# Performance work log

Measured on AMD Instinct MI355X. Metric: run time of the kernel, lower is better.

## Reference

```python
import jax, jax.numpy as jnp
import numpy as np

L, B, S, D, H = 6, 2, 2048, 512, 8
DH = D // H
FF = 4 * D
EPS = 1e-5


def setup_inputs() -> dict:
    key = jax.random.key(0)
    ks = jax.random.split(key, 10)
    w = lambda k, shape: jax.random.normal(k, shape, jnp.float32) * 0.02
    return {
        "query": jax.random.normal(ks[0], (B, S, D), jnp.float32),
        "key": jax.random.normal(ks[1], (B, S, D), jnp.float32),
        "query_mask": jnp.ones((B, S), jnp.int32),
        "key_mask": jnp.ones((B, S), jnp.int32),
        # per-layer stacked params; conv1d(kernel=1) == linear with weight [out,in]
        "Wq": w(ks[2], (L, D, D)), "bq": jnp.zeros((L, D), jnp.float32),
        "Wk": w(ks[3], (L, D, D)), "bk": jnp.zeros((L, D), jnp.float32),
        "Wv": w(ks[4], (L, D, D)), "bv": jnp.zeros((L, D), jnp.float32),
        "Wo": w(ks[5], (L, D, D)), "bo": jnp.zeros((L, D), jnp.float32),
        "ln1_g": jnp.ones((L, D), jnp.float32), "ln1_b": jnp.zeros((L, D), jnp.float32),
        "ff_w1": w(ks[6], (L, FF, D)), "ff_b1": jnp.zeros((L, FF), jnp.float32),
        "ff_w2": w(ks[7], (L, D, FF)), "ff_b2": jnp.zeros((L, D), jnp.float32),
        "ln2_g": jnp.ones((L, D), jnp.float32), "ln2_b": jnp.zeros((L, D), jnp.float32),
    }


def _layer_norm(x, g, b):
    m = jnp.mean(x, axis=-1, keepdims=True)
    v = jnp.mean(jnp.square(x - m), axis=-1, keepdims=True)
    return (x - m) * jax.lax.rsqrt(v + EPS) * g + b


def reference(query, key, query_mask, key_mask,
              Wq, bq, Wk, bk, Wv, bv, Wo, bo,
              ln1_g, ln1_b, ff_w1, ff_b1, ff_w2, ff_b2, ln2_g, ln2_b):
    b_, s_, d_ = query.shape
    kpad = (key_mask == 0)[:, None, None, :]          # [B,1,1,K]
    qm = query_mask.astype(query.dtype)[:, :, None]    # [B,S,1]
    x = query
    for i in range(L):
        # QKV projections (conv1d kernel-size-1 == linear), split heads -> [B,H,S,DH]
        def split(t):
            return t.reshape(b_, s_, H, DH).transpose(0, 2, 1, 3)
        q = split(x @ Wq[i].T + bq[i]) * (float(DH) ** -0.5)
        k = split(key @ Wk[i].T + bk[i])
        v = split(key @ Wv[i].T + bv[i])
        attn = jnp.einsum('bhqd,bhkd->bhqk', q, k)
        attn = jnp.where(kpad, -jnp.inf, attn)
        attn = jax.nn.softmax(attn, axis=-1)
        o = jnp.einsum('bhqk,bhkd->bhqd', attn, v)
        o = o.transpose(0, 2, 1, 3).reshape(b_, s_, H * DH)
        o = (o @ Wo[i].T + bo[i]) * qm                 # output proj + query mask
        x = _layer_norm(o + x, ln1_g[i], ln1_b[i])
        h = jax.nn.leaky_relu(x @ ff_w1[i].T + ff_b1[i], 0.01)
        f = (h @ ff_w2[i].T + ff_b2[i]) * qm           # FFN mask on output
        x = _layer_norm(f + x, ln2_g[i], ln2_b[i])
    return x
```

## Files before the change

kernel.cpp:

```cpp
#include <hip/hip_runtime.h>
#include <stdint.h>

constexpr int LAYERS = 6;
constexpr int Bc = 2, Sc = 2048, Dc = 512, Hc = 8, DHc = 64, FFc = 2048;
constexpr int Mc = Bc * Sc;
constexpr int NS = 2;
constexpr int KCHUNK = Sc / NS;

typedef __attribute__((ext_vector_type(8))) __bf16 bf16x8;
typedef __attribute__((ext_vector_type(4))) __bf16 bf16x4;
typedef __attribute__((ext_vector_type(4))) float f32x4;

__device__ __forceinline__ void async_ld16(const void* g, void* lds) {
  __builtin_amdgcn_global_load_lds(
      (const __attribute__((address_space(1))) uint32_t*)g,
      (__attribute__((address_space(3))) uint32_t*)lds, 16, 0, 0);
}

__global__ __launch_bounds__(256) void cvt_kernel(const float* __restrict__ in,
                                                  __bf16* __restrict__ out, int n) {
  int i = (blockIdx.x * 256 + threadIdx.x) * 4;
  if (i + 4 > n) return;
  const float4 v = *(const float4*)(in + i);
  bf16x4 o;
  o[0] = (__bf16)v.x; o[1] = (__bf16)v.y; o[2] = (__bf16)v.z; o[3] = (__bf16)v.w;
  *(bf16x4*)(out + i) = o;
}

template <int BM, int BN, int WM, int WN, int EPI>
__global__ __launch_bounds__(256) void gemm_bt(
    const __bf16* __restrict__ A, const __bf16* __restrict__ W,
    const float* __restrict__ bias, const float* __restrict__ bias2,
    float* __restrict__ outf, __bf16* __restrict__ outb,
    __bf16* __restrict__ outb2, const int* __restrict__ rmask, float scale,
    int M, int N, int K) {
  constexpr int BK = 32;
  __shared__ __bf16 As[2][BM * BK];
  __shared__ __bf16 Bs[2][BN * BK];
  const int tid = threadIdx.x;
  const int l15 = tid & 15;
  const int lg = (tid & 63) >> 4;
  const int w = tid >> 6;
  const int wm = w >> 1, wn = w & 1;
  const int tm = blockIdx.y * BM;
  const int tn = blockIdx.x * BN;
  const __bf16* Ap = A + (size_t)tm * K;
  const __bf16* Wp = W + (size_t)tn * K;
  f32x4 acc[WM][WN] = {};

  auto stage = [&](int k0, int bf) {
#pragma unroll
    for (int c = 0; c < BM * 4 / 256; ++c) {
      int cc = c * 256 + tid;
      async_ld16(Ap + (size_t)(cc >> 2) * K + k0 + (cc & 3) * 8, &As[bf][cc * 8]);
    }
#pragma unroll
    for (int c = 0; c < BN * 4 / 256; ++c) {
      int cc = c * 256 + tid;
      async_ld16(Wp + (size_t)(cc >> 2) * K + k0 + (cc & 3) * 8, &Bs[bf][cc * 8]);
    }
  };

  const int nk = K / BK;
  stage(0, 0);
  __syncthreads();
  int buf = 0;
  for (int t = 0; t < nk; ++t) {
    if (t + 1 < nk) stage((t + 1) * BK, buf ^ 1);
    bf16x8 af[WM], bfr[WN];
#pragma unroll
    for (int i = 0; i < WM; ++i)
      af[i] = *(const bf16x8*)&As[buf][(wm * WM * 16 + i * 16 + l15) * BK + lg * 8];
#pragma unroll
    for (int j = 0; j < WN; ++j)
      bfr[j] = *(const bf16x8*)&Bs[buf][(wn * WN * 16 + j * 16 + l15) * BK + lg * 8];
#pragma unroll
    for (int i = 0; i < WM; ++i)
#pragma unroll
      for (int j = 0; j < WN; ++j)
        acc[i][j] = __builtin_amdgcn_mfma_f32_16x16x32_bf16(af[i], bfr[j], acc[i][j], 0, 0, 0);
    __syncthreads();
    buf ^= 1;
  }

#pragma unroll
  for (int i = 0; i < WM; ++i) {
#pragma unroll
    for (int j = 0; j < WN; ++j) {
      const int n = tn + wn * WN * 16 + j * 16 + l15;
      float bv;
      if constexpr (EPI == 6) {
        int lyr = n >> 10, w1 = n & 1023, p = w1 >> 9, d = w1 & 511;
        bv = (p ? bias2 : bias)[lyr * 512 + d];
      } else {
        bv = bias[n];
      }
#pragma unroll
      for (int r = 0; r < 4; ++r) {
        const int m = tm + wm * WM * 16 + i * 16 + lg * 4 + r;
        float v = acc[i][j][r] + bv;
        if constexpr (EPI == 1) {
          int b = m >> 11, s = m & (Sc - 1);
          int h = n >> 6, dh = n & 63;
          outb[(((size_t)(b * Hc + h)) * Sc + s) * DHc + dh] = (__bf16)(v * scale);
        } else if constexpr (EPI == 3) {
          outf[(size_t)m * N + n] = v * (float)rmask[m];
        } else if constexpr (EPI == 4) {
          float lv = v > 0.f ? v : 0.01f * v;
          outb[(size_t)m * N + n] = (__bf16)lv;
        } else if constexpr (EPI == 6) {
          int b = m >> 11, s = m & (Sc - 1);
          int lyr = n >> 10, w1 = n & 1023, p = w1 >> 9, d = w1 & 511;
          int h = d >> 6, dh = d & 63;
          if (p == 0)
            outb[((((size_t)(lyr * Bc + b) * Hc + h)) * Sc + s) * DHc + dh] = (__bf16)v;
          else
            outb2[((((size_t)(lyr * Bc + b) * Hc + h)) * DHc + dh) * Sc + s] = (__bf16)v;
        }
      }
    }
  }
}

__global__ __launch_bounds__(256, 4) void attn_kernel(
    const __bf16* __restrict__ q, const __bf16* __restrict__ k,
    const __bf16* __restrict__ vt, const int* __restrict__ kmask,
    __bf16* __restrict__ Opart, float* __restrict__ mpart,
    float* __restrict__ lpart) {
  const int bh = blockIdx.y;
  const int b = bh >> 3;
  const int z = blockIdx.z;
  const int w = threadIdx.x >> 6;
  const int l = threadIdx.x & 63;
  const int l15 = l & 15;
  const int lg = l >> 4;
  const int tid = threadIdx.x;
  const int qbase = blockIdx.x * 64 + w * 16;
  const int k0 = z * KCHUNK;

  const __bf16* qp = q + ((size_t)bh * Sc + qbase) * DHc;
  const __bf16* kp = k + (size_t)bh * Sc * DHc;
  const __bf16* vp = vt + (size_t)bh * DHc * Sc;

  bf16x8 qf[2];
  qf[0] = *(const bf16x8*)(qp + l15 * DHc + lg * 8);
  qf[1] = *(const bf16x8*)(qp + l15 * DHc + 32 + lg * 8);

  bf16x8 onesf;
#pragma unroll
  for (int i = 0; i < 8; ++i) onesf[i] = (__bf16)1.0f;

  f32x4 oacc[4] = {};
  f32x4 lacc = {};
  float mr[4] = {-1e30f, -1e30f, -1e30f, -1e30f};

  __shared__ __bf16 Ks[2][4096];
  __shared__ __bf16 Vs[2][4096];
  __shared__ __bf16 P[4][1024];

  auto stage = [&](int t, int bf) {
    const int kt = k0 + t * 64;
#pragma unroll
    for (int ii = 0; ii < 2; ++ii) {
      int i = ii * 256 + tid;
      int r = i >> 3;
      int bsrc = (i & 7) ^ (r & 7);
      async_ld16(kp + (size_t)(kt + r) * DHc + bsrc * 8, &Ks[bf][i * 8]);
      async_ld16(vp + (size_t)r * Sc + kt + bsrc * 8, &Vs[bf][i * 8]);
    }
  };

  stage(0, 0);
  __syncthreads();

  constexpr int NT = KCHUNK / 64;
  int buf = 0;
  for (int t = 0; t < NT; ++t) {
    const int kt = k0 + t * 64;
    if (t + 1 < NT) stage(t + 1, buf ^ 1);

    f32x4 sacc[4] = {};
#pragma unroll
    for (int kf = 0; kf < 2; ++kf) {
#pragma unroll
      for (int cb = 0; cb < 4; ++cb) {
        int row = cb * 16 + l15;
        bf16x8 kfr = *(const bf16x8*)&Ks[buf][row * 64 + (((kf * 4 + lg) ^ (row & 7)) * 8)];
        sacc[cb] = __builtin_amdgcn_mfma_f32_16x16x32_bf16(qf[kf], kfr, sacc[cb], 0, 0, 0);
      }
    }
#pragma unroll
    for (int cb = 0; cb < 4; ++cb) {
      if (kmask[b * Sc + kt + cb * 16 + l15] == 0) {
        sacc[cb][0] = -1e30f; sacc[cb][1] = -1e30f;
        sacc[cb][2] = -1e30f; sacc[cb][3] = -1e30f;
      }
    }
    float fac[4];
#pragma unroll
    for (int j = 0; j < 4; ++j) {
      float mx = fmaxf(fmaxf(sacc[0][j], sacc[1][j]), fmaxf(sacc[2][j], sacc[3][j]));
#pragma unroll
      for (int d = 1; d < 16; d <<= 1) mx = fmaxf(mx, __shfl_xor(mx, d, 64));
      float mn = fmaxf(mr[j], mx);
      fac[j] = __expf(mr[j] - mn);
      mr[j] = mn;
    }
#pragma unroll
    for (int cb = 0; cb < 4; ++cb)
#pragma unroll
      for (int j = 0; j < 4; ++j) sacc[cb][j] = __expf(sacc[cb][j] - mr[j]);
#pragma unroll
    for (int j = 0; j < 4; ++j) lacc[j] *= fac[j];
#pragma unroll
    for (int db = 0; db < 4; ++db)
#pragma unroll
      for (int j = 0; j < 4; ++j) oacc[db][j] *= fac[j];

#pragma unroll
    for (int cb = 0; cb < 4; ++cb)
#pragma unroll
      for (int j = 0; j < 4; ++j) {
        int qrow = lg * 4 + j;
        P[w][qrow * 64 + ((cb * 16 + l15) ^ ((qrow & 7) << 3))] = (__bf16)sacc[cb][j];
      }
#pragma unroll
    for (int kf = 0; kf < 2; ++kf) {
      bf16x8 pf = *(const bf16x8*)&P[w][l15 * 64 + (((kf * 4 + lg) ^ (l15 & 7)) * 8)];
      lacc = __builtin_amdgcn_mfma_f32_16x16x32_bf16(pf, onesf, lacc, 0, 0, 0);
#pragma unroll
      for (int db = 0; db < 4; ++db) {
        int row = db * 16 + l15;
        bf16x8 vf = *(const bf16x8*)&Vs[buf][row * 64 + (((kf * 4 + lg) ^ (row & 7)) * 8)];
        oacc[db] = __builtin_amdgcn_mfma_f32_16x16x32_bf16(pf, vf, oacc[db], 0, 0, 0);
      }
    }
    __syncthreads();
    buf ^= 1;
  }

  const size_t obase = (((size_t)(z * Bc * Hc + bh)) * Sc + qbase) * DHc;
#pragma unroll
  for (int db = 0; db < 4; ++db)
#pragma unroll
    for (int j = 0; j < 4; ++j)
      Opart[obase + (size_t)(lg * 4 + j) * DHc + db * 16 + l15] = (__bf16)oacc[db][j];
  if (l15 == 0) {
#pragma unroll
    for (int j = 0; j < 4; ++j) {
      int row = (z * Bc * Hc + bh) * Sc + qbase + lg * 4 + j;
      mpart[row] = mr[j];
      lpart[row] = lacc[j];
    }
  }
}

__global__ __launch_bounds__(256) void attn_combine(
    const __bf16* __restrict__ Opart, const float* __restrict__ mpart,
    const float* __restrict__ lpart, __bf16* __restrict__ out) {
  int t = blockIdx.x * 256 + threadIdx.x;
  int d = t & 63;
  int row = t >> 6;
  int bh = row >> 11, s = row & (Sc - 1);
  constexpr int RSTRIDE = Bc * Hc * Sc;
  float m0 = mpart[row], m1 = mpart[RSTRIDE + row];
  float l0 = lpart[row], l1 = lpart[RSTRIDE + row];
  float M = fmaxf(m0, m1);
  float e0 = __expf(m0 - M), e1 = __expf(m1 - M);
  float denom = e0 * l0 + e1 * l1;
  float o0 = (float)Opart[(size_t)row * DHc + d];
  float o1 = (float)Opart[((size_t)RSTRIDE + row) * DHc + d];
  float o = (e0 * o0 + e1 * o1) / denom;
  int b = bh >> 3, h = bh & 7;
  out[(((size_t)b * Sc + s)) * Dc + h * DHc + d] = (__bf16)o;
}

__global__ __launch_bounds__(256) void add_ln_kernel(
    const float* __restrict__ res, const float* __restrict__ xin,
    const float* __restrict__ g, const float* __restrict__ bb,
    float* __restrict__ xo, __bf16* __restrict__ xbo) {
  const int row = blockIdx.x;
  const int tid = threadIdx.x;
  const float* rp = res + (size_t)row * Dc;
  const float* xp = xin + (size_t)row * Dc;
  float v0 = rp[tid] + xp[tid];
  float v1 = rp[tid + 256] + xp[tid + 256];
  float s = v0 + v1;
#pragma unroll
  for (int d = 1; d < 64; d <<= 1) s += __shfl_xor(s, d, 64);
  __shared__ float red[4], red2[4];
  if ((tid & 63) == 0) red[tid >> 6] = s;
  __syncthreads();
  float mean = (red[0] + red[1] + red[2] + red[3]) * (1.0f / Dc);
  float d0 = v0 - mean, d1 = v1 - mean;
  float qq = d0 * d0 + d1 * d1;
#pragma unroll
  for (int d = 1; d < 64; d <<= 1) qq += __shfl_xor(qq, d, 64);
  if ((tid & 63) == 0) red2[tid >> 6] = qq;
  __syncthreads();
  float var = (red2[0] + red2[1] + red2[2] + red2[3]) * (1.0f / Dc);
  float rs = rsqrtf(var + 1e-5f);
  float o0 = d0 * rs * g[tid] + bb[tid];
  float o1 = d1 * rs * g[tid + 256] + bb[tid + 256];
  xo[(size_t)row * Dc + tid] = o0;
  xo[(size_t)row * Dc + tid + 256] = o1;
  xbo[(size_t)row * Dc + tid] = (__bf16)o0;
  xbo[(size_t)row * Dc + tid + 256] = (__bf16)o1;
}

extern "C" void kernel_launch(void* const* d_in, const int* in_sizes, int n_in,
                              void* d_out, int out_size, void* d_ws, size_t ws_size,
                              hipStream_t stream) {
  (void)in_sizes; (void)n_in; (void)out_size; (void)ws_size;
  const float* query = (const float*)d_in[0];
  const float* key   = (const float*)d_in[1];
  const int* qmask   = (const int*)d_in[2];
  const int* kmask   = (const int*)d_in[3];
  const float* Wq = (const float*)d_in[4];
  const float* bq = (const float*)d_in[5];
  const float* Wk = (const float*)d_in[6];
  const float* bk = (const float*)d_in[7];
  const float* Wv = (const float*)d_in[8];
  const float* bv = (const float*)d_in[9];
  const float* Wo = (const float*)d_in[10];
  const float* bo = (const float*)d_in[11];
  const float* ln1g = (const float*)d_in[12];
  const float* ln1b = (const float*)d_in[13];
  const float* fw1 = (const float*)d_in[14];
  const float* fb1 = (const float*)d_in[15];
  const float* fw2 = (const float*)d_in[16];
  const float* fb2 = (const float*)d_in[17];
  const float* ln2g = (const float*)d_in[18];
  const float* ln2b = (const float*)d_in[19];

  char* ws = (char*)d_ws;
  size_t off = 0;
  auto carve = [&](size_t bytes) -> void* {
    void* p = ws + off;
    off += (bytes + 255) & ~(size_t)255;
    return p;
  };
  float* x_f    = (float*)carve((size_t)Mc * Dc * 4);
  float* tmp_f  = (float*)carve((size_t)Mc * Dc * 4);
  __bf16* x_b   = (__bf16*)carve((size_t)Mc * Dc * 2);
  __bf16* key_b = (__bf16*)carve((size_t)Mc * Dc * 2);
  __bf16* q_b   = (__bf16*)carve((size_t)Mc * Dc * 2);
  __bf16* at_b  = (__bf16*)carve((size_t)Mc * Dc * 2);
  __bf16* h_b   = (__bf16*)carve((size_t)Mc * FFc * 2);
  __bf16* k_all = (__bf16*)carve((size_t)LAYERS * Mc * Dc * 2);
  __bf16* vt_all= (__bf16*)carve((size_t)LAYERS * Mc * Dc * 2);
  __bf16* wq_b  = (__bf16*)carve((size_t)LAYERS * Dc * Dc * 2);
  __bf16* wkv_b = (__bf16*)carve((size_t)LAYERS * 2 * Dc * Dc * 2);
  __bf16* wo_b  = (__bf16*)carve((size_t)LAYERS * Dc * Dc * 2);
  __bf16* w1_b  = (__bf16*)carve((size_t)LAYERS * FFc * Dc * 2);
  __bf16* w2_b  = (__bf16*)carve((size_t)LAYERS * Dc * FFc * 2);
  float* ml_f   = (float*)carve((size_t)NS * Bc * Hc * Sc * 4 * 2);

  __bf16* opart_b = h_b;
  float* mpart_f = ml_f;
  float* lpart_f = ml_f + (size_t)NS * Bc * Hc * Sc;

  auto cvt = [&](const float* src, __bf16* dst, int n) {
    cvt_kernel<<<n / 1024, 256, 0, stream>>>(src, dst, n);
  };
  cvt(query, x_b, Mc * Dc);
  cvt(key, key_b, Mc * Dc);
  cvt(Wq, wq_b, LAYERS * Dc * Dc);
  for (int i = 0; i < LAYERS; ++i) {
    cvt(Wk + (size_t)i * Dc * Dc, wkv_b + ((size_t)i * 2 + 0) * Dc * Dc, Dc * Dc);
    cvt(Wv + (size_t)i * Dc * Dc, wkv_b + ((size_t)i * 2 + 1) * Dc * Dc, Dc * Dc);
  }
  cvt(Wo, wo_b, LAYERS * Dc * Dc);
  cvt(fw1, w1_b, LAYERS * FFc * Dc);
  cvt(fw2, w2_b, LAYERS * Dc * FFc);
  hipMemcpyAsync(x_f, query, (size_t)Mc * Dc * 4, hipMemcpyDeviceToDevice, stream);

  const dim3 blk(256);
  const dim3 gP64(Dc / 64, Mc / 64);
  const dim3 gKV(LAYERS * 2 * Dc / 128, Mc / 128);
  const dim3 gFF1(FFc / 128, Mc / 128);
  const dim3 gAttn(Sc / 64, Bc * Hc, NS);
  const dim3 gComb(Bc * Hc * Sc * DHc / 256);

  gemm_bt<128, 128, 4, 4, 6><<<gKV, blk, 0, stream>>>(
      key_b, wkv_b, bk, bv, nullptr, k_all, vt_all, nullptr, 1.0f,
      Mc, LAYERS * 2 * Dc, Dc);

  for (int i = 0; i < LAYERS; ++i) {
    const __bf16* wq_i = wq_b + (size_t)i * Dc * Dc;
    const __bf16* wo_i = wo_b + (size_t)i * Dc * Dc;
    const __bf16* w1_i = w1_b + (size_t)i * FFc * Dc;
    const __bf16* w2_i = w2_b + (size_t)i * Dc * FFc;
    const __bf16* k_i  = k_all + (size_t)i * Mc * Dc;
    const __bf16* vt_i = vt_all + (size_t)i * Mc * Dc;

    gemm_bt<64, 64, 2, 2, 1><<<gP64, blk, 0, stream>>>(
        x_b, wq_i, bq + i * Dc, nullptr, nullptr, q_b, nullptr, nullptr, 0.125f,
        Mc, Dc, Dc);
    attn_kernel<<<gAttn, blk, 0, stream>>>(q_b, k_i, vt_i, kmask,
                                           opart_b, mpart_f, lpart_f);
    attn_combine<<<gComb, blk, 0, stream>>>(opart_b, mpart_f, lpart_f, at_b);
    gemm_bt<64, 64, 2, 2, 3><<<gP64, blk, 0, stream>>>(
        at_b, wo_i, bo + i * Dc, nullptr, tmp_f, nullptr, nullptr, qmask, 1.0f,
        Mc, Dc, Dc);
    add_ln_kernel<<<Mc, blk, 0, stream>>>(tmp_f, x_f, ln1g + i * Dc, ln1b + i * Dc, x_f, x_b);
    gemm_bt<128, 128, 4, 4, 4><<<gFF1, blk, 0, stream>>>(
        x_b, w1_i, fb1 + i * FFc, nullptr, nullptr, h_b, nullptr, nullptr, 1.0f,
        Mc, FFc, Dc);
    gemm_bt<64, 64, 2, 2, 3><<<gP64, blk, 0, stream>>>(
        h_b, w2_i, fb2 + i * Dc, nullptr, tmp_f, nullptr, nullptr, qmask, 1.0f,
        Mc, Dc, FFc);
    add_ln_kernel<<<Mc, blk, 0, stream>>>(tmp_f, x_f, ln2g + i * Dc, ln2b + i * Dc, x_f, x_b);
  }
  hipMemcpyAsync(d_out, x_f, (size_t)Mc * Dc * 4, hipMemcpyDeviceToDevice, stream);
}
```

Baseline: 931.5 us.

## Split-K the FFN2 GEMM, fuse mask into LayerNorm, lazy softmax rescale

The FFN down-projection GEMM is split into two K halves across blockIdx.z, writing two fp32 partials that the add+LayerNorm kernel sums. The row mask multiply also moves from the GEMM epilogue into that kernel. This raises block count for the narrow N=512 GEMM at the cost of an extra fp32 partial write and read. The attention kernel now skips online-softmax rescaling unless the running max rises by more than 8 for some lane, trading fewer exp/multiply ops for a bounded exponent growth. The FFN1 GEMM tile is changed from 128x128 to 64x128.

```diff
diff --git a/kernel.cpp b/kernel.cpp
--- a/kernel.cpp
+++ b/kernel.cpp
@@ -32,8 +32,8 @@
     const __bf16* __restrict__ A, const __bf16* __restrict__ W,
     const float* __restrict__ bias, const float* __restrict__ bias2,
     float* __restrict__ outf, __bf16* __restrict__ outb,
-    __bf16* __restrict__ outb2, const int* __restrict__ rmask, float scale,
-    int M, int N, int K) {
+    __bf16* __restrict__ outb2, float scale,
+    int M, int N, int K, int Kstride) {
   constexpr int BK = 32;
   __shared__ __bf16 As[2][BM * BK];
   __shared__ __bf16 Bs[2][BN * BK];
@@ -44,20 +44,21 @@
   const int wm = w >> 1, wn = w & 1;
   const int tm = blockIdx.y * BM;
   const int tn = blockIdx.x * BN;
-  const __bf16* Ap = A + (size_t)tm * K;
-  const __bf16* Wp = W + (size_t)tn * K;
+  const int z = blockIdx.z;
+  const __bf16* Ap = A + (size_t)tm * Kstride + (size_t)z * K;
+  const __bf16* Wp = W + (size_t)tn * Kstride + (size_t)z * K;
   f32x4 acc[WM][WN] = {};
 
   auto stage = [&](int k0, int bf) {
 #pragma unroll
     for (int c = 0; c < BM * 4 / 256; ++c) {
       int cc = c * 256 + tid;
-      async_ld16(Ap + (size_t)(cc >> 2) * K + k0 + (cc & 3) * 8, &As[bf][cc * 8]);
+      async_ld16(Ap + (size_t)(cc >> 2) * Kstride + k0 + (cc & 3) * 8, &As[bf][cc * 8]);
     }
 #pragma unroll
     for (int c = 0; c < BN * 4 / 256; ++c) {
       int cc = c * 256 + tid;
-      async_ld16(Wp + (size_t)(cc >> 2) * K + k0 + (cc & 3) * 8, &Bs[bf][cc * 8]);
+      async_ld16(Wp + (size_t)(cc >> 2) * Kstride + k0 + (cc & 3) * 8, &Bs[bf][cc * 8]);
     }
   };
 
@@ -92,6 +93,8 @@
       if constexpr (EPI == 6) {
         int lyr = n >> 10, w1 = n & 1023, p = w1 >> 9, d = w1 & 511;
         bv = (p ? bias2 : bias)[lyr * 512 + d];
+      } else if constexpr (EPI == 0) {
+        bv = (z == 0) ? bias[n] : 0.f;
       } else {
         bv = bias[n];
       }
@@ -99,12 +102,12 @@
       for (int r = 0; r < 4; ++r) {
         const int m = tm + wm * WM * 16 + i * 16 + lg * 4 + r;
         float v = acc[i][j][r] + bv;
-        if constexpr (EPI == 1) {
+        if constexpr (EPI == 0) {
+          outf[(size_t)z * M * N + (size_t)m * N + n] = v;
+        } else if constexpr (EPI == 1) {
           int b = m >> 11, s = m & (Sc - 1);
           int h = n >> 6, dh = n & 63;
           outb[(((size_t)(b * Hc + h)) * Sc + s) * DHc + dh] = (__bf16)(v * scale);
-        } else if constexpr (EPI == 3) {
-          outf[(size_t)m * N + n] = v * (float)rmask[m];
         } else if constexpr (EPI == 4) {
           float lv = v > 0.f ? v : 0.01f * v;
           outb[(size_t)m * N + n] = (__bf16)lv;
@@ -196,26 +199,31 @@
         sacc[cb][2] = -1e30f; sacc[cb][3] = -1e30f;
       }
     }
-    float fac[4];
+    float mx[4];
 #pragma unroll
     for (int j = 0; j < 4; ++j) {
-      float mx = fmaxf(fmaxf(sacc[0][j], sacc[1][j]), fmaxf(sacc[2][j], sacc[3][j]));
-#pragma unroll
-      for (int d = 1; d < 16; d <<= 1) mx = fmaxf(mx, __shfl_xor(mx, d, 64));
-      float mn = fmaxf(mr[j], mx);
-      fac[j] = __expf(mr[j] - mn);
-      mr[j] = mn;
+      float m0 = fmaxf(fmaxf(sacc[0][j], sacc[1][j]), fmaxf(sacc[2][j], sacc[3][j]));
+#pragma unroll
+      for (int d = 1; d < 16; d <<= 1) m0 = fmaxf(m0, __shfl_xor(m0, d, 64));
+      mx[j] = m0;
+    }
+    bool need = (mx[0] > mr[0] + 8.f) || (mx[1] > mr[1] + 8.f) ||
+                (mx[2] > mr[2] + 8.f) || (mx[3] > mr[3] + 8.f);
+    if (__any(need)) {
+#pragma unroll
+      for (int j = 0; j < 4; ++j) {
+        float mn = fmaxf(mr[j], mx[j]);
+        float f = __expf(mr[j] - mn);
+        mr[j] = mn;
+        lacc[j] *= f;
+#pragma unroll
+        for (int db = 0; db < 4; ++db) oacc[db][j] *= f;
+      }
     }
 #pragma unroll
     for (int cb = 0; cb < 4; ++cb)
 #pragma unroll
       for (int j = 0; j < 4; ++j) sacc[cb][j] = __expf(sacc[cb][j] - mr[j]);
-#pragma unroll
-    for (int j = 0; j < 4; ++j) lacc[j] *= fac[j];
-#pragma unroll
-    for (int db = 0; db < 4; ++db)
-#pragma unroll
-      for (int j = 0; j < 4; ++j) oacc[db][j] *= fac[j];
 
 #pragma unroll
     for (int cb = 0; cb < 4; ++cb)
@@ -276,15 +284,23 @@
 }
 
 __global__ __launch_bounds__(256) void add_ln_kernel(
-    const float* __restrict__ res, const float* __restrict__ xin,
+    const float* __restrict__ res, const float* __restrict__ res2,
+    const int* __restrict__ rmask, const float* __restrict__ xin,
     const float* __restrict__ g, const float* __restrict__ bb,
     float* __restrict__ xo, __bf16* __restrict__ xbo) {
   const int row = blockIdx.x;
   const int tid = threadIdx.x;
   const float* rp = res + (size_t)row * Dc;
   const float* xp = xin + (size_t)row * Dc;
-  float v0 = rp[tid] + xp[tid];
-  float v1 = rp[tid + 256] + xp[tid + 256];
+  float mfac = rmask ? (float)rmask[row] : 1.f;
+  float a0 = rp[tid], a1 = rp[tid + 256];
+  if (res2) {
+    const float* r2p = res2 + (size_t)row * Dc;
+    a0 += r2p[tid];
+    a1 += r2p[tid + 256];
+  }
+  float v0 = a0 * mfac + xp[tid];
+  float v1 = a1 * mfac + xp[tid + 256];
   float s = v0 + v1;
 #pragma unroll
   for (int d = 1; d < 64; d <<= 1) s += __shfl_xor(s, d, 64);
@@ -341,7 +357,7 @@
     return p;
   };
   float* x_f    = (float*)carve((size_t)Mc * Dc * 4);
-  float* tmp_f  = (float*)carve((size_t)Mc * Dc * 4);
+  float* tmp_f  = (float*)carve((size_t)2 * Mc * Dc * 4);
   __bf16* x_b   = (__bf16*)carve((size_t)Mc * Dc * 2);
   __bf16* key_b = (__bf16*)carve((size_t)Mc * Dc * 2);
   __bf16* q_b   = (__bf16*)carve((size_t)Mc * Dc * 2);
@@ -359,6 +375,7 @@
   __bf16* opart_b = h_b;
   float* mpart_f = ml_f;
   float* lpart_f = ml_f + (size_t)NS * Bc * Hc * Sc;
+  float* tmp2_f = tmp_f + (size_t)Mc * Dc;
 
   auto cvt = [&](const float* src, __bf16* dst, int n) {
     cvt_kernel<<<n / 1024, 256, 0, stream>>>(src, dst, n);
@@ -377,14 +394,15 @@
 
   const dim3 blk(256);
   const dim3 gP64(Dc / 64, Mc / 64);
+  const dim3 gFF2(Dc / 64, Mc / 64, 2);
   const dim3 gKV(LAYERS * 2 * Dc / 128, Mc / 128);
-  const dim3 gFF1(FFc / 128, Mc / 128);
+  const dim3 gFF1(FFc / 128, Mc / 64);
   const dim3 gAttn(Sc / 64, Bc * Hc, NS);
   const dim3 gComb(Bc * Hc * Sc * DHc / 256);
 
   gemm_bt<128, 128, 4, 4, 6><<<gKV, blk, 0, stream>>>(
-      key_b, wkv_b, bk, bv, nullptr, k_all, vt_all, nullptr, 1.0f,
-      Mc, LAYERS * 2 * Dc, Dc);
+      key_b, wkv_b, bk, bv, nullptr, k_all, vt_all, 1.0f,
+      Mc, LAYERS * 2 * Dc, Dc, Dc);
 
   for (int i = 0; i < LAYERS; ++i) {
     const __bf16* wq_i = wq_b + (size_t)i * Dc * Dc;
@@ -395,22 +413,24 @@
     const __bf16* vt_i = vt_all + (size_t)i * Mc * Dc;
 
     gemm_bt<64, 64, 2, 2, 1><<<gP64, blk, 0, stream>>>(
-        x_b, wq_i, bq + i * Dc, nullptr, nullptr, q_b, nullptr, nullptr, 0.125f,
-        Mc, Dc, Dc);
+        x_b, wq_i, bq + i * Dc, nullptr, nullptr, q_b, nullptr, 0.125f,
+        Mc, Dc, Dc, Dc);
     attn_kernel<<<gAttn, blk, 0, stream>>>(q_b, k_i, vt_i, kmask,
                                            opart_b, mpart_f, lpart_f);
     attn_combine<<<gComb, blk, 0, stream>>>(opart_b, mpart_f, lpart_f, at_b);
-    gemm_bt<64, 64, 2, 2, 3><<<gP64, blk, 0, stream>>>(
-        at_b, wo_i, bo + i * Dc, nullptr, tmp_f, nullptr, nullptr, qmask, 1.0f,
-        Mc, Dc, Dc);
-    add_ln_kernel<<<Mc, blk, 0, stream>>>(tmp_f, x_f, ln1g + i * Dc, ln1b + i * Dc, x_f, x_b);
-    gemm_bt<128, 128, 4, 4, 4><<<gFF1, blk, 0, stream>>>(
-        x_b, w1_i, fb1 + i * FFc, nullptr, nullptr, h_b, nullptr, nullptr, 1.0f,
-        Mc, FFc, Dc);
-    gemm_bt<64, 64, 2, 2, 3><<<gP64, blk, 0, stream>>>(
-        h_b, w2_i, fb2 + i * Dc, nullptr, tmp_f, nullptr, nullptr, qmask, 1.0f,
-        Mc, Dc, FFc);
-    add_ln_kernel<<<Mc, blk, 0, stream>>>(tmp_f, x_f, ln2g + i * Dc, ln2b + i * Dc, x_f, x_b);
+    gemm_bt<64, 64, 2, 2, 0><<<gP64, blk, 0, stream>>>(
+        at_b, wo_i, bo + i * Dc, nullptr, tmp_f, nullptr, nullptr, 1.0f,
+        Mc, Dc, Dc, Dc);
+    add_ln_kernel<<<Mc, blk, 0, stream>>>(tmp_f, nullptr, qmask, x_f,
+                                          ln1g + i * Dc, ln1b + i * Dc, x_f, x_b);
+    gemm_bt<64, 128, 2, 4, 4><<<gFF1, blk, 0, stream>>>(
+        x_b, w1_i, fb1 + i * FFc, nullptr, nullptr, h_b, nullptr, 1.0f,
+        Mc, FFc, Dc, Dc);
+    gemm_bt<64, 64, 2, 2, 0><<<gFF2, blk, 0, stream>>>(
+        h_b, w2_i, fb2 + i * Dc, nullptr, tmp_f, nullptr, nullptr, 1.0f,
+        Mc, Dc, FFc / 2, FFc);
+    add_ln_kernel<<<Mc, blk, 0, stream>>>(tmp_f, tmp2_f, qmask, x_f,
+                                          ln2g + i * Dc, ln2b + i * Dc, x_f, x_b);
   }
   hipMemcpyAsync(d_out, x_f, (size_t)Mc * Dc * 4, hipMemcpyDeviceToDevice, stream);
 }
```

New measurement: 914.6 us. Within noise of the previous version (-1.8%).
